# Kernel tuning notes

Hardware: AMD Instinct MI355X
Metric: run time of the kernel (lower is better)

Reference implementation:

```python
import jax, jax.numpy as jnp
import numpy as np
from jax import lax

P = 128   # patch_size
S = 64    # stride
K = 31    # PSF kernel size
NZ = 15   # number of Zernike coefficients
HID = 64  # aberration MLP hidden width


def setup_inputs() -> dict:
    key = jax.random.key(0)
    ks = jax.random.split(key, 8)
    B, C, H, W = 8, 3, 512, 512
    x_hat = jax.random.uniform(ks[0], (B, C, H, W), dtype=jnp.float32)
    w1 = jax.random.normal(ks[1], (2, HID), dtype=jnp.float32) * 0.5
    b1 = jnp.zeros((HID,), jnp.float32)
    w2 = jax.random.normal(ks[2], (HID, HID), dtype=jnp.float32) * 0.125
    b2 = jnp.zeros((HID,), jnp.float32)
    w3 = jax.random.normal(ks[3], (HID, NZ), dtype=jnp.float32) * 0.1
    b3 = jnp.zeros((NZ,), jnp.float32)
    zernike_basis = jax.random.normal(ks[4], (NZ, K, K), dtype=jnp.float32) * 0.5
    return {"x_hat": x_hat, "w1": w1, "b1": b1, "w2": w2, "b2": b2,
            "w3": w3, "b3": b3, "zernike_basis": zernike_basis}


def _hann(n):
    # torch.hann_window (periodic=True): 0.5*(1 - cos(2*pi*k/n))
    return 0.5 - 0.5 * jnp.cos(2.0 * jnp.pi * jnp.arange(n, dtype=jnp.float32) / n)


def _psf_from_coeffs(coeffs, basis):
    # coeffs: [N, NZ], basis: [NZ, K, K] -> normalized PSFs [N, K, K]
    phase = jnp.einsum('nz,zhw->nhw', coeffs, basis)          # [N, K, K]
    g = jnp.linspace(-1.0, 1.0, K, dtype=jnp.float32)
    r2 = g[:, None] ** 2 + g[None, :] ** 2
    mask = (r2 <= 1.0).astype(jnp.float32)                    # circular pupil
    pupil = mask * jnp.exp(1j * phase.astype(jnp.complex64))
    field = jnp.fft.fftshift(jnp.fft.fft2(jnp.fft.ifftshift(pupil, axes=(-2, -1))), axes=(-2, -1))
    psf = jnp.abs(field) ** 2
    psf = psf / (jnp.sum(psf, axis=(-2, -1), keepdims=True) + 1e-12)
    return psf


def _forward(x_hat, w1, b1, w2, b2, w3, b3, basis):
    B, C, H, W = x_hat.shape
    pad_h = (S - (H - P) % S) % S
    pad_w = (S - (W - P) % S) % S
    x = jnp.pad(x_hat, ((0, 0), (0, 0), (0, pad_h), (0, pad_w)), mode='reflect') \
        if (pad_h or pad_w) else x_hat
    H_pad, W_pad = x.shape[2], x.shape[3]
    n_h = (H_pad - P) // S + 1
    n_w = (W_pad - P) // S + 1
    N = n_h * n_w

    # ---- unfold into overlapping patches: [B*N, C, P, P] ----
    r0 = jnp.arange(n_h) * S
    c0 = jnp.arange(n_w) * S
    ridx = r0[:, None] + jnp.arange(P)[None, :]               # [n_h, P]
    cidx = c0[:, None] + jnp.arange(P)[None, :]               # [n_w, P]
    patches = x[:, :, ridx[:, None, :, None], cidx[None, :, None, :]]  # [B,C,n_h,n_w,P,P]
    patches = patches.transpose(0, 2, 3, 1, 4, 5).reshape(B * N, C, P, P)

    # ---- per-patch normalized center coords in [-1, 1] ----
    y_norm = (r0.astype(jnp.float32) + P / 2.0) / H_pad * 2.0 - 1.0
    x_norm = (c0.astype(jnp.float32) + P / 2.0) / W_pad * 2.0 - 1.0
    gy, gx = jnp.meshgrid(y_norm, x_norm, indexing='ij')
    coords = jnp.stack([gy, gx], axis=-1).reshape(N, 2)       # [N, 2]
    coords = jnp.tile(coords, (B, 1))                         # [B*N, 2]

    # ---- aberration MLP -> Zernike coeffs -> PSF kernels ----
    h = jax.nn.relu(coords @ w1 + b1)
    h = jax.nn.relu(h @ w2 + b2)
    coeffs = h @ w3 + b3                                      # [B*N, NZ]
    psf = _psf_from_coeffs(coeffs, basis)                     # [B*N, K, K], C_k = 1
    kf = psf[:, ::-1, ::-1]                                   # flip -> true convolution

    # ---- spatially varying per-patch conv (C>1, C_k==1 broadcast branch) ----
    BN = B * N
    pad = K // 2
    xp = jnp.pad(patches, ((0, 0), (0, 0), (pad, pad), (pad, pad)))
    lhs = xp.reshape(1, BN * C, P + 2 * pad, P + 2 * pad)
    rhs = jnp.broadcast_to(kf[:, None, :, :], (BN, C, K, K)).reshape(BN * C, 1, K, K)
    y = lax.conv_general_dilated(lhs, rhs, (1, 1), 'VALID',
                                 dimension_numbers=('NCHW', 'OIHW', 'NCHW'),
                                 feature_group_count=BN * C)
    y_patches = y.reshape(BN, C, P, P)

    # ---- Hann window + overlap-add fold ----
    hann = _hann(P)
    window = hann[:, None] * hann[None, :]                    # [P, P]
    y_patches = y_patches * window[None, None]

    idx = (ridx[:, None, :, None] * W_pad + cidx[None, :, None, :]).reshape(-1)  # [N*P*P]
    vals = y_patches.reshape(B, N, C, P, P).transpose(0, 2, 1, 3, 4).reshape(B, C, -1)
    y_accum = jnp.zeros((B, C, H_pad * W_pad), jnp.float32).at[:, :, idx].add(vals)
    y_accum = y_accum.reshape(B, C, H_pad, W_pad)

    wvals = jnp.broadcast_to(window, (N, P, P)).reshape(-1)
    w_accum = jnp.zeros((H_pad * W_pad,), jnp.float32).at[idx].add(wvals)
    w_accum = w_accum.reshape(1, 1, H_pad, W_pad)

    y_hat = y_accum / (w_accum + 1e-8)
    return y_hat[:, :, :H, :W]


def reference(x_hat, w1, b1, w2, b2, w3, b3, zernike_basis):
    return _forward(x_hat, w1, b1, w2, b2, w3, b3, zernike_basis)
```

## Files before the change

kernel.cpp:

```cpp
#include <hip/hip_runtime.h>
#include <math.h>

#define B_ 8
#define C_ 3
#define HW_ 512
#define P_ 128
#define S_ 64
#define K_ 31
#define NZ_ 15
#define HID_ 64
#define NPOS_ 49
#define BN_ (B_*NPOS_)

#define LSTRIDE_ 168
#define TROWS_ 160
#define FRAG_U32_ 256
#define NSTEP_ 16
#define BPOS_U32_ (NSTEP_ * 3 * FRAG_U32_)

typedef __attribute__((ext_vector_type(8))) short bf16x8;
typedef __attribute__((ext_vector_type(4))) float f32x4;

__device__ __forceinline__ float hann128(int p) {
    return 0.5f - 0.5f * cosf(6.283185307179586f * (float)p / 128.0f);
}

__device__ __forceinline__ unsigned short bf16_rne(float f) {
    union { float f; unsigned int u; } v; v.f = f;
    unsigned int r = v.u + 0x7fffu + ((v.u >> 16) & 1u);
    return (unsigned short)(r >> 16);
}

__device__ __forceinline__ float bf16_to_f(unsigned int bits16) {
    union { unsigned int u; float f; } v; v.u = bits16 << 16;
    return v.f;
}

__global__ __launch_bounds__(1024) void psf_kernel(
    const float* __restrict__ w1, const float* __restrict__ b1,
    const float* __restrict__ w2, const float* __restrict__ b2,
    const float* __restrict__ w3, const float* __restrict__ b3,
    const float* __restrict__ basis, unsigned int* __restrict__ bfrags)
{
    __shared__ float h1[HID_], h2[HID_], coef[NZ_];
    __shared__ float pupR[961], pupI[961], tR[961], tI[961];
    __shared__ float rootR[31], rootI[31];
    __shared__ float red[16];
    int n = blockIdx.x;
    int nh = n / 7, nw = n % 7;
    int tid = threadIdx.x;
    float cy = (float)(nh * S_ + P_ / 2) * (2.0f / (float)HW_) - 1.0f;
    float cx = (float)(nw * S_ + P_ / 2) * (2.0f / (float)HW_) - 1.0f;

    if (tid < HID_) h1[tid] = fmaxf(0.0f, cy * w1[tid] + cx * w1[HID_ + tid] + b1[tid]);
    if (tid < 31) {
        float ang = -6.283185307179586f * (float)tid / 31.0f;
        rootR[tid] = cosf(ang);
        rootI[tid] = sinf(ang);
    }
    __syncthreads();
    if (tid < HID_) {
        float s = b2[tid];
        for (int k = 0; k < HID_; ++k) s = fmaf(h1[k], w2[k * HID_ + tid], s);
        h2[tid] = fmaxf(0.0f, s);
    }
    __syncthreads();
    if (tid < NZ_) {
        float s = b3[tid];
        for (int k = 0; k < HID_; ++k) s = fmaf(h2[k], w3[k * NZ_ + tid], s);
        coef[tid] = s;
    }
    __syncthreads();

    for (int idx = tid; idx < 961; idx += 1024) {
        int h = idx / 31, w = idx % 31;
        float ph = 0.0f;
        for (int z = 0; z < NZ_; ++z) ph = fmaf(coef[z], basis[z * 961 + idx], ph);
        int dh = h - 15, dw = w - 15;
        bool m = (dh * dh + dw * dw) <= 225;
        float sv, cv;
        sincosf(ph, &sv, &cv);
        pupR[idx] = m ? cv : 0.0f;
        pupI[idx] = m ? sv : 0.0f;
    }
    __syncthreads();

    for (int idx = tid; idx < 961; idx += 1024) {
        int h = idx / 31, k = idx % 31;
        float ar = 0.0f, ai = 0.0f;
        for (int w = 0; w < 31; ++w) {
            int tt = (k * w) % 31;
            float cr = rootR[tt], ci = rootI[tt];
            float pr = pupR[h * 31 + w], pi = pupI[h * 31 + w];
            ar += pr * cr - pi * ci;
            ai += pr * ci + pi * cr;
        }
        tR[idx] = ar; tI[idx] = ai;
    }
    __syncthreads();

    float lsum = 0.0f;
    for (int idx = tid; idx < 961; idx += 1024) {
        int u = idx / 31, k = idx % 31;
        float gr = 0.0f, gi = 0.0f;
        for (int h = 0; h < 31; ++h) {
            int tt = (u * h) % 31;
            float cr = rootR[tt], ci = rootI[tt];
            float ar = tR[h * 31 + k], ai = tI[h * 31 + k];
            gr += ar * cr - ai * ci;
            gi += ar * ci + ai * cr;
        }
        float p = gr * gr + gi * gi;
        pupR[idx] = p;
        lsum += p;
    }
    float v = lsum;
    #pragma unroll
    for (int off = 32; off >= 1; off >>= 1) v += __shfl_xor(v, off, 64);
    if ((tid & 63) == 0) red[tid >> 6] = v;
    __syncthreads();
    if (tid == 0) {
        float s = 0.0f;
        #pragma unroll
        for (int i = 0; i < 16; ++i) s += red[i];
        red[0] = 1.0f / (s + 1e-12f);
    }
    __syncthreads();
    float inv = red[0];
    for (int idx = tid; idx < 961; idx += 1024) {
        int j = idx / 31, i = idx % 31;
        int u = (15 - j + 31) % 31, vv = (15 - i + 31) % 31;
        tI[idx] = pupR[u * 31 + vv] * inv;
    }
    __syncthreads();

    unsigned int* bf = bfrags + (size_t)n * BPOS_U32_;
    for (int w2 = tid; w2 < BPOS_U32_; w2 += 1024) {
        int jc = w2 >> 8;
        int s = jc / 3, c = jc % 3;
        int rem = w2 & 255;
        int l = rem >> 2, ew = rem & 3;
        int nn = l & 15, kg = l >> 4;
        unsigned int pack = 0;
        #pragma unroll
        for (int q = 0; q < 2; ++q) {
            int e = ew * 2 + q;
            int kk = kg * 8 + e;
            int jrow = 2 * s + (kk >> 4);
            int tap = 16 * c + (kk & 15) - nn;
            float vx = (jrow <= 30 && tap >= 0 && tap <= 30) ? tI[jrow * 31 + tap] : 0.0f;
            pack |= (unsigned int)bf16_rne(vx) << (16 * q);
        }
        bf[w2] = pack;
    }
}

template<int MODE>
__global__ __launch_bounds__(1024, 8) void conv_mfma_kernel(
    const float* __restrict__ x, const unsigned int* __restrict__ bfrags,
    void* __restrict__ dst)
{
    __shared__ unsigned short sIn[TROWS_ * LSTRIDE_];
    __shared__ float sH[128];

    int t = blockIdx.x;
    int cc = t % 3;
    int bn = t / 3;
    int b = bn / NPOS_, n = bn % NPOS_;
    int nh = n / 7, nw = n % 7;
    int r0 = nh * S_, c0 = nw * S_;
    int tid = threadIdx.x;

    if (tid < 128) sH[tid] = hann128(tid);

    const float* xb = x + ((size_t)(b * C_ + cc) * HW_ + r0) * HW_ + c0;
    for (int i = tid; i < TROWS_ * 40; i += 1024) {
        int r = i / 40, c4 = (i % 40) * 4;
        bool rv = (r >= 15 && r < 143);
        unsigned int pk[2] = {0, 0};
        #pragma unroll
        for (int q = 0; q < 4; ++q) {
            int c = c4 + q;
            float v = 0.0f;
            if (rv && c >= 15 && c < 143) v = xb[(r - 15) * HW_ + (c - 15)];
            pk[q >> 1] |= (unsigned int)bf16_rne(v) << (16 * (q & 1));
        }
        *(uint2*)&sIn[r * LSTRIDE_ + c4] = make_uint2(pk[0], pk[1]);
    }
    __syncthreads();

    int lane = tid & 63, wv = tid >> 6;
    int m0 = (wv & 7) * 16;
    int ch = (wv >> 3) * 64;
    int lrow = lane & 15, lkg = lane >> 4;

    f32x4 acc[4];
    #pragma unroll
    for (int q = 0; q < 4; ++q) acc[q] = (f32x4){0.f, 0.f, 0.f, 0.f};

    int abase = (m0 + lrow + (lkg >> 1)) * (LSTRIDE_ * 2) + ch * 2 + (lkg & 1) * 16;
    const bf16x8* bpos = (const bf16x8*)(bfrags + (size_t)n * BPOS_U32_) + lane;

    bf16x8 Bc0 = bpos[0], Bc1 = bpos[64], Bc2 = bpos[128];

    #pragma unroll 2
    for (int s = 0; s < NSTEP_; ++s) {
        bf16x8 Bn0, Bn1, Bn2;
        if (s + 1 < NSTEP_) {
            const bf16x8* bnp = bpos + (s + 1) * 192;
            Bn0 = bnp[0]; Bn1 = bnp[64]; Bn2 = bnp[128];
        } else {
            Bn0 = Bc0; Bn1 = Bc1; Bn2 = Bc2;
        }
        const char* ap = (const char*)sIn + abase;
        bf16x8 A[6];
        #pragma unroll
        for (int p = 0; p < 6; ++p) A[p] = *(const bf16x8*)(ap + p * 32);
        #pragma unroll
        for (int q = 0; q < 4; ++q) {
            acc[q] = __builtin_amdgcn_mfma_f32_16x16x32_bf16(A[q],     Bc0, acc[q], 0, 0, 0);
            acc[q] = __builtin_amdgcn_mfma_f32_16x16x32_bf16(A[q + 1], Bc1, acc[q], 0, 0, 0);
            acc[q] = __builtin_amdgcn_mfma_f32_16x16x32_bf16(A[q + 2], Bc2, acc[q], 0, 0, 0);
        }
        Bc0 = Bn0; Bc1 = Bn1; Bc2 = Bn2;
        abase += 2 * (LSTRIDE_ * 2);
    }

    float hy[4];
    #pragma unroll
    for (int r = 0; r < 4; ++r) hy[r] = sH[m0 + lkg * 4 + r];

    #pragma unroll
    for (int q = 0; q < 4; ++q) {
        int xloc = ch + 16 * q + lrow;
        float hxv = sH[xloc];
        #pragma unroll
        for (int r = 0; r < 4; ++r) {
            int yloc = m0 + lkg * 4 + r;
            float val = acc[q][r] * hy[r] * hxv;
            if (MODE == 0) {
                unsigned short* yp = (unsigned short*)dst + (((size_t)bn * C_ + cc) << 14);
                yp[yloc * P_ + xloc] = bf16_rne(val);
            } else {
                float* ob = (float*)dst;
                atomicAdd(ob + ((size_t)(b * C_ + cc) * HW_ + r0 + yloc) * HW_ + c0 + xloc, val);
            }
        }
    }
}

__global__ __launch_bounds__(256) void gather_kernel(
    const unsigned short* __restrict__ ypatch, float* __restrict__ out)
{
    __shared__ float sH[128];
    int tid = threadIdx.x;
    if (tid < 128) sH[tid] = hann128(tid);
    __syncthreads();

    int gid = blockIdx.x * 256 + tid;
    int base = gid * 4;
    if (base >= B_ * C_ * HW_ * HW_) return;
    int X = base & 511;
    int Y = (base >> 9) & 511;
    int bc = base >> 18;
    int c = bc % 3, b = bc / 3;
    int nhA = Y >> 6, pyA = Y & 63;
    int nwA = X >> 6, pxA = X & 63;
    bool vA = nhA <= 6, vB = nhA >= 1;
    bool uA = nwA <= 6, uB = nwA >= 1;
    float wy = (vA ? sH[pyA] : 0.0f) + (vB ? sH[pyA + 64] : 0.0f);

    float4 acc = {0.f, 0.f, 0.f, 0.f};
    #pragma unroll
    for (int sy = 0; sy < 2; ++sy) {
        bool okY = sy == 0 ? vA : vB;
        int nh = sy == 0 ? nhA : nhA - 1;
        int py = sy == 0 ? pyA : pyA + 64;
        #pragma unroll
        for (int sx = 0; sx < 2; ++sx) {
            bool okX = sx == 0 ? uA : uB;
            int nw = sx == 0 ? nwA : nwA - 1;
            int px = sx == 0 ? pxA : pxA + 64;
            if (okY && okX) {
                size_t off = ((((size_t)b * NPOS_ + nh * 7 + nw) * C_ + c) << 14) + (py << 7) + px;
                uint2 v = *(const uint2*)&ypatch[off];
                acc.x += bf16_to_f(v.x & 0xffffu);
                acc.y += bf16_to_f(v.x >> 16);
                acc.z += bf16_to_f(v.y & 0xffffu);
                acc.w += bf16_to_f(v.y >> 16);
            }
        }
    }
    float4 o;
    float wx0 = (uA ? sH[pxA + 0] : 0.0f) + (uB ? sH[pxA + 64] : 0.0f);
    float wx1 = (uA ? sH[pxA + 1] : 0.0f) + (uB ? sH[pxA + 65] : 0.0f);
    float wx2 = (uA ? sH[pxA + 2] : 0.0f) + (uB ? sH[pxA + 66] : 0.0f);
    float wx3 = (uA ? sH[pxA + 3] : 0.0f) + (uB ? sH[pxA + 67] : 0.0f);
    o.x = acc.x / (wy * wx0 + 1e-8f);
    o.y = acc.y / (wy * wx1 + 1e-8f);
    o.z = acc.z / (wy * wx2 + 1e-8f);
    o.w = acc.w / (wy * wx3 + 1e-8f);
    *(float4*)&out[base] = o;
}

__global__ __launch_bounds__(256) void divide_kernel(float* __restrict__ out)
{
    int idx = blockIdx.x * 256 + threadIdx.x;
    if (idx >= B_ * C_ * HW_ * HW_) return;
    int X = idx & 511;
    int Y = (idx >> 9) & 511;
    int nhA = Y >> 6, pyA = Y & 63;
    int nwA = X >> 6, pxA = X & 63;
    float wy = (nhA <= 6 ? hann128(pyA) : 0.0f) + (nhA >= 1 ? hann128(pyA + 64) : 0.0f);
    float wx = (nwA <= 6 ? hann128(pxA) : 0.0f) + (nwA >= 1 ? hann128(pxA + 64) : 0.0f);
    out[idx] = out[idx] / (wy * wx + 1e-8f);
}

extern "C" void kernel_launch(void* const* d_in, const int* in_sizes, int n_in,
                              void* d_out, int out_size, void* d_ws, size_t ws_size,
                              hipStream_t stream)
{
    const float* x    = (const float*)d_in[0];
    const float* w1   = (const float*)d_in[1];
    const float* b1   = (const float*)d_in[2];
    const float* w2   = (const float*)d_in[3];
    const float* b2   = (const float*)d_in[4];
    const float* w3   = (const float*)d_in[5];
    const float* b3   = (const float*)d_in[6];
    const float* basis = (const float*)d_in[7];
    float* out = (float*)d_out;

    unsigned int* bfrags = (unsigned int*)d_ws;
    size_t bfBytes = (size_t)NPOS_ * BPOS_U32_ * sizeof(unsigned int);
    size_t need = bfBytes + (size_t)BN_ * C_ * P_ * P_ * sizeof(unsigned short);

    psf_kernel<<<NPOS_, 1024, 0, stream>>>(w1, b1, w2, b2, w3, b3, basis, bfrags);

    int nPix = B_ * C_ * HW_ * HW_;
    if (ws_size >= need) {
        unsigned short* ypatch = (unsigned short*)((char*)d_ws + bfBytes);
        conv_mfma_kernel<0><<<BN_ * C_, 1024, 0, stream>>>(x, bfrags, ypatch);
        gather_kernel<<<(nPix / 4 + 255) / 256, 256, 0, stream>>>(ypatch, out);
    } else {
        hipMemsetAsync(d_out, 0, (size_t)out_size * sizeof(float), stream);
        conv_mfma_kernel<1><<<BN_ * C_, 1024, 0, stream>>>(x, bfrags, out);
        divide_kernel<<<(nPix + 255) / 256, 256, 0, stream>>>(out);
    }
}
```

Measured before the change: 87.80 us.

## Split conv patch into row halves with vectorized staging and prefetched A fragments

Each patch-channel convolution block is split into two 512-thread blocks, each covering 64 output rows, which shrinks the shared input tile from 160 to 96 rows. The input is zero-filled, then loaded with float4 reads at a 16-element offset, and the PSF fragment layout is shifted by one tap to match that alignment. The MFMA loop now double-buffers the A fragments from LDS alongside the B prefetch. The intent is to cut LDS footprint, raise occupancy and vectorize global loads, at the cost of loading the halo rows twice and adding a zero-fill pass.

New measurement: 86.12 us. About the same (-1.9%).

```diff
diff --git a/kernel.cpp b/kernel.cpp
--- a/kernel.cpp
+++ b/kernel.cpp
@@ -13,7 +13,7 @@
 #define BN_ (B_*NPOS_)
 
 #define LSTRIDE_ 168
-#define TROWS_ 160
+#define TROWS_ 96
 #define FRAG_U32_ 256
 #define NSTEP_ 16
 #define BPOS_U32_ (NSTEP_ * 3 * FRAG_U32_)
@@ -148,7 +148,8 @@
             int kk = kg * 8 + e;
             int jrow = 2 * s + (kk >> 4);
             int tap = 16 * c + (kk & 15) - nn;
-            float vx = (jrow <= 30 && tap >= 0 && tap <= 30) ? tI[jrow * 31 + tap] : 0.0f;
+            float vx = (jrow >= 1 && jrow <= 31 && tap >= 1 && tap <= 31)
+                       ? tI[(jrow - 1) * 31 + (tap - 1)] : 0.0f;
             pack |= (unsigned int)bf16_rne(vx) << (16 * q);
         }
         bf[w2] = pack;
@@ -156,7 +157,7 @@
 }
 
 template<int MODE>
-__global__ __launch_bounds__(1024, 8) void conv_mfma_kernel(
+__global__ __launch_bounds__(512, 4) void conv_mfma_kernel(
     const float* __restrict__ x, const unsigned int* __restrict__ bfrags,
     void* __restrict__ dst)
 {
@@ -164,8 +165,9 @@
     __shared__ float sH[128];
 
     int t = blockIdx.x;
-    int cc = t % 3;
-    int bn = t / 3;
+    int half = t & 1;
+    int cc = (t >> 1) % 3;
+    int bn = t / 6;
     int b = bn / NPOS_, n = bn % NPOS_;
     int nh = n / 7, nw = n % 7;
     int r0 = nh * S_, c0 = nw * S_;
@@ -173,25 +175,27 @@
 
     if (tid < 128) sH[tid] = hann128(tid);
 
+    for (int i = tid; i < TROWS_ * LSTRIDE_ * 2 / 16; i += 512)
+        ((uint4*)sIn)[i] = make_uint4(0u, 0u, 0u, 0u);
+    __syncthreads();
+
     const float* xb = x + ((size_t)(b * C_ + cc) * HW_ + r0) * HW_ + c0;
-    for (int i = tid; i < TROWS_ * 40; i += 1024) {
-        int r = i / 40, c4 = (i % 40) * 4;
-        bool rv = (r >= 15 && r < 143);
-        unsigned int pk[2] = {0, 0};
-        #pragma unroll
-        for (int q = 0; q < 4; ++q) {
-            int c = c4 + q;
-            float v = 0.0f;
-            if (rv && c >= 15 && c < 143) v = xb[(r - 15) * HW_ + (c - 15)];
-            pk[q >> 1] |= (unsigned int)bf16_rne(v) << (16 * (q & 1));
-        }
-        *(uint2*)&sIn[r * LSTRIDE_ + c4] = make_uint2(pk[0], pk[1]);
+    int rpbase = half * 64 - 16;
+    for (int i = tid; i < TROWS_ * 32; i += 512) {
+        int r = i >> 5, c4 = (i & 31) * 4;
+        int rp = rpbase + r;
+        if (rp >= 0 && rp < P_) {
+            float4 v = *(const float4*)&xb[rp * HW_ + c4];
+            unsigned int lo = (unsigned int)bf16_rne(v.x) | ((unsigned int)bf16_rne(v.y) << 16);
+            unsigned int hi = (unsigned int)bf16_rne(v.z) | ((unsigned int)bf16_rne(v.w) << 16);
+            *(uint2*)&sIn[r * LSTRIDE_ + 16 + c4] = make_uint2(lo, hi);
+        }
     }
     __syncthreads();
 
     int lane = tid & 63, wv = tid >> 6;
-    int m0 = (wv & 7) * 16;
-    int ch = (wv >> 3) * 64;
+    int m0 = (wv & 3) * 16;
+    int ch = (wv >> 2) * 64;
     int lrow = lane & 15, lkg = lane >> 4;
 
     f32x4 acc[4];
@@ -201,49 +205,60 @@
     int abase = (m0 + lrow + (lkg >> 1)) * (LSTRIDE_ * 2) + ch * 2 + (lkg & 1) * 16;
     const bf16x8* bpos = (const bf16x8*)(bfrags + (size_t)n * BPOS_U32_) + lane;
 
+    bf16x8 Ac[6];
+    {
+        const char* ap = (const char*)sIn + abase;
+        #pragma unroll
+        for (int p = 0; p < 6; ++p) Ac[p] = *(const bf16x8*)(ap + p * 32);
+    }
     bf16x8 Bc0 = bpos[0], Bc1 = bpos[64], Bc2 = bpos[128];
 
-    #pragma unroll 2
-    for (int s = 0; s < NSTEP_; ++s) {
-        bf16x8 Bn0, Bn1, Bn2;
-        if (s + 1 < NSTEP_) {
-            const bf16x8* bnp = bpos + (s + 1) * 192;
-            Bn0 = bnp[0]; Bn1 = bnp[64]; Bn2 = bnp[128];
-        } else {
-            Bn0 = Bc0; Bn1 = Bc1; Bn2 = Bc2;
-        }
+    #pragma unroll 3
+    for (int s = 0; s < NSTEP_ - 1; ++s) {
+        abase += 2 * (LSTRIDE_ * 2);
+        bf16x8 An[6];
         const char* ap = (const char*)sIn + abase;
-        bf16x8 A[6];
-        #pragma unroll
-        for (int p = 0; p < 6; ++p) A[p] = *(const bf16x8*)(ap + p * 32);
+        #pragma unroll
+        for (int p = 0; p < 6; ++p) An[p] = *(const bf16x8*)(ap + p * 32);
+        const bf16x8* bnp = bpos + (s + 1) * 192;
+        bf16x8 Bn0 = bnp[0], Bn1 = bnp[64], Bn2 = bnp[128];
+
         #pragma unroll
         for (int q = 0; q < 4; ++q) {
-            acc[q] = __builtin_amdgcn_mfma_f32_16x16x32_bf16(A[q],     Bc0, acc[q], 0, 0, 0);
-            acc[q] = __builtin_amdgcn_mfma_f32_16x16x32_bf16(A[q + 1], Bc1, acc[q], 0, 0, 0);
-            acc[q] = __builtin_amdgcn_mfma_f32_16x16x32_bf16(A[q + 2], Bc2, acc[q], 0, 0, 0);
-        }
+            acc[q] = __builtin_amdgcn_mfma_f32_16x16x32_bf16(Ac[q],     Bc0, acc[q], 0, 0, 0);
+            acc[q] = __builtin_amdgcn_mfma_f32_16x16x32_bf16(Ac[q + 1], Bc1, acc[q], 0, 0, 0);
+            acc[q] = __builtin_amdgcn_mfma_f32_16x16x32_bf16(Ac[q + 2], Bc2, acc[q], 0, 0, 0);
+        }
+        #pragma unroll
+        for (int p = 0; p < 6; ++p) Ac[p] = An[p];
         Bc0 = Bn0; Bc1 = Bn1; Bc2 = Bn2;
-        abase += 2 * (LSTRIDE_ * 2);
-    }
-
+    }
+    #pragma unroll
+    for (int q = 0; q < 4; ++q) {
+        acc[q] = __builtin_amdgcn_mfma_f32_16x16x32_bf16(Ac[q],     Bc0, acc[q], 0, 0, 0);
+        acc[q] = __builtin_amdgcn_mfma_f32_16x16x32_bf16(Ac[q + 1], Bc1, acc[q], 0, 0, 0);
+        acc[q] = __builtin_amdgcn_mfma_f32_16x16x32_bf16(Ac[q + 2], Bc2, acc[q], 0, 0, 0);
+    }
+
+    int prow0 = half * 64 + m0 + lkg * 4;
     float hy[4];
     #pragma unroll
-    for (int r = 0; r < 4; ++r) hy[r] = sH[m0 + lkg * 4 + r];
+    for (int r = 0; r < 4; ++r) hy[r] = sH[prow0 + r];
 
     #pragma unroll
     for (int q = 0; q < 4; ++q) {
-        int xloc = ch + 16 * q + lrow;
-        float hxv = sH[xloc];
+        int pcol = ch + 16 * q + lrow;
+        float hxv = sH[pcol];
         #pragma unroll
         for (int r = 0; r < 4; ++r) {
-            int yloc = m0 + lkg * 4 + r;
+            int prow = prow0 + r;
             float val = acc[q][r] * hy[r] * hxv;
             if (MODE == 0) {
                 unsigned short* yp = (unsigned short*)dst + (((size_t)bn * C_ + cc) << 14);
-                yp[yloc * P_ + xloc] = bf16_rne(val);
+                yp[prow * P_ + pcol] = bf16_rne(val);
             } else {
                 float* ob = (float*)dst;
-                atomicAdd(ob + ((size_t)(b * C_ + cc) * HW_ + r0 + yloc) * HW_ + c0 + xloc, val);
+                atomicAdd(ob + ((size_t)(b * C_ + cc) * HW_ + r0 + prow) * HW_ + c0 + pcol, val);
             }
         }
     }
@@ -339,11 +354,11 @@
     int nPix = B_ * C_ * HW_ * HW_;
     if (ws_size >= need) {
         unsigned short* ypatch = (unsigned short*)((char*)d_ws + bfBytes);
-        conv_mfma_kernel<0><<<BN_ * C_, 1024, 0, stream>>>(x, bfrags, ypatch);
+        conv_mfma_kernel<0><<<BN_ * C_ * 2, 512, 0, stream>>>(x, bfrags, ypatch);
         gather_kernel<<<(nPix / 4 + 255) / 256, 256, 0, stream>>>(ypatch, out);
     } else {
         hipMemsetAsync(d_out, 0, (size_t)out_size * sizeof(float), stream);
-        conv_mfma_kernel<1><<<BN_ * C_, 1024, 0, stream>>>(x, bfrags, out);
+        conv_mfma_kernel<1><<<BN_ * C_ * 2, 512, 0, stream>>>(x, bfrags, out);
         divide_kernel<<<(nPix + 255) / 256, 256, 0, stream>>>(out);
     }
 }
```
